# Performance work log

Hardware: AMD Instinct MI355X
Metric: run time of the kernel (lower is better)

The kernel has to match this reference:

```python
import jax, jax.numpy as jnp
import numpy as np

N_NODES = 50000


def setup_inputs() -> dict:
    key = jax.random.key(0)
    k1, k2, k3, k4, k5 = jax.random.split(key, 5)
    x = jax.random.normal(k1, (N_NODES, 128), dtype=jnp.float32)
    edge_index = jax.random.randint(k2, (2, 800000), 0, N_NODES, dtype=jnp.int64)
    # Linear layers: torch Linear stores weight as [out, in]; init ~ U(-1/sqrt(in), 1/sqrt(in))
    s = 1.0 / np.sqrt(128.0)
    W_rel = jax.random.uniform(k3, (128, 128), dtype=jnp.float32, minval=-s, maxval=s)
    b_rel = jax.random.uniform(k4, (128,), dtype=jnp.float32, minval=-s, maxval=s)
    W_root = jax.random.uniform(k5, (128, 128), dtype=jnp.float32, minval=-s, maxval=s)
    return {"x": x, "edge_index": edge_index, "W_rel": W_rel, "b_rel": b_rel, "W_root": W_root}


def reference(x, edge_index, W_rel, b_rel, W_root):
    # GraphConv (PyG): out_i = W_rel @ (sum_{j -> i} x_j) + b_rel + W_root @ x_i
    src, dst = edge_index[0], edge_index[1]
    msgs = x[src]  # [E, in] gather
    agg = jax.ops.segment_sum(msgs, dst, num_segments=N_NODES)  # [N, in] scatter-add
    out = agg @ W_rel.T + b_rel + x @ W_root.T
    # ReLU; dropout_rate = DropoutRate.NONE -> p=0, identity
    return jax.nn.relu(out)
```

## Files before the change

kernel.cpp:

```cpp
#include <hip/hip_runtime.h>
#include <hip/hip_bf16.h>


#define F 128
#define NPB 32
#define NPARTS 8
#define CAPLOG 7
#define CAP (1 << CAPLOG)
#define CAPB 768
#define SCAN_CHUNK 2048

typedef __bf16 bf16x8 __attribute__((ext_vector_type(8)));
typedef float f32x4 __attribute__((ext_vector_type(4)));

__device__ inline unsigned f32_to_bf16_rne(float f) {
  unsigned u = __float_as_uint(f);
  unsigned r = u + 0x7fffu + ((u >> 16) & 1u);
  return r >> 16;
}

__global__ __launch_bounds__(256) void convert_bf16_kernel(
    const float2* __restrict__ in, unsigned* __restrict__ out, int n2) {
  int i = blockIdx.x * blockDim.x + threadIdx.x;
  int stride = gridDim.x * blockDim.x;
  for (; i < n2; i += stride) {
    float2 v = in[i];
    out[i] = f32_to_bf16_rne(v.x) | (f32_to_bf16_rne(v.y) << 16);
  }
}

__global__ __launch_bounds__(256) void bin_kernel(
    const int* __restrict__ ei, int* __restrict__ binCursor,
    unsigned* __restrict__ bin, int E, int NB) {
  const int part = blockIdx.x & (NPARTS - 1);
  const int stride = gridDim.x * blockDim.x;
  for (int e = blockIdx.x * blockDim.x + threadIdx.x; e < E; e += stride) {
    unsigned src = (unsigned)ei[e];
    unsigned dst = (unsigned)ei[E + e];
    unsigned key = (dst << 16) | src;
    int cell = part * NB + (int)(dst >> 5);
    int slot = atomicAdd(&binCursor[cell], 1);
    if (slot < CAP) bin[((size_t)cell << CAPLOG) + slot] = key;
  }
}

__global__ __launch_bounds__(256) void agg_sort_kernel(
    const unsigned* __restrict__ xb, const unsigned* __restrict__ bin,
    const int* __restrict__ binCursor, unsigned* __restrict__ aggb,
    int N, int NB) {
  __shared__ int cntS[NPB];
  __shared__ int offS[NPB];
  __shared__ int curS[NPB];
  __shared__ unsigned short eLds[CAPB];
  const int b = blockIdx.x;
  const int t = threadIdx.x;

  if (t < NPB) cntS[t] = 0;
  __syncthreads();

  unsigned kreg[NPARTS];
  int cnt_p[NPARTS];
#pragma unroll
  for (int p = 0; p < NPARTS; ++p) {
    int cell = p * NB + b;
    int c = min(binCursor[cell], CAP);
    cnt_p[p] = c;
    if (t < c) {
      kreg[p] = bin[((size_t)cell << CAPLOG) + t];
      atomicAdd(&cntS[(kreg[p] >> 16) & (NPB - 1)], 1);
    }
  }
  __syncthreads();

  if (t < 64) {
    int v = (t < NPB) ? cntS[t] : 0;
    int incl = v;
#pragma unroll
    for (int off = 1; off < NPB; off <<= 1) {
      int u = __shfl_up(incl, off);
      if (t >= off) incl += u;
    }
    if (t < NPB) {
      offS[t] = incl - v;
      curS[t] = incl - v;
    }
  }
  __syncthreads();

#pragma unroll
  for (int p = 0; p < NPARTS; ++p) {
    if (t < cnt_p[p]) {
      int d = (kreg[p] >> 16) & (NPB - 1);
      int pos = atomicAdd(&curS[d], 1);
      if (pos < CAPB) eLds[pos] = (unsigned short)(kreg[p] & 0xffffu);
    }
  }
  __syncthreads();

  const int wave = t >> 6;
  const int lane = t & 63;
  const int nodeBase = b * NPB;
  for (int di = wave; di < NPB; di += 4) {
    int node = nodeBase + di;
    if (node >= N) continue;
    int beg = min(offS[di], CAPB);
    int end = min(offS[di] + cntS[di], CAPB);
    float ax = 0.f, ay = 0.f;
    int e = beg;
    for (; e + 3 < end; e += 4) {
      int s0 = eLds[e + 0];
      int s1 = eLds[e + 1];
      int s2 = eLds[e + 2];
      int s3 = eLds[e + 3];
      unsigned v0 = xb[(size_t)s0 * 64 + lane];
      unsigned v1 = xb[(size_t)s1 * 64 + lane];
      unsigned v2 = xb[(size_t)s2 * 64 + lane];
      unsigned v3 = xb[(size_t)s3 * 64 + lane];
      ax += __uint_as_float(v0 << 16);
      ay += __uint_as_float(v0 & 0xffff0000u);
      ax += __uint_as_float(v1 << 16);
      ay += __uint_as_float(v1 & 0xffff0000u);
      ax += __uint_as_float(v2 << 16);
      ay += __uint_as_float(v2 & 0xffff0000u);
      ax += __uint_as_float(v3 << 16);
      ay += __uint_as_float(v3 & 0xffff0000u);
    }
    for (; e < end; ++e) {
      unsigned v = xb[(size_t)eLds[e] * 64 + lane];
      ax += __uint_as_float(v << 16);
      ay += __uint_as_float(v & 0xffff0000u);
    }
    aggb[(size_t)node * 64 + lane] = f32_to_bf16_rne(ax) | (f32_to_bf16_rne(ay) << 16);
  }
}

__global__ __launch_bounds__(256) void gemm_mfma_kernel(
    const __bf16* __restrict__ aggb, const __bf16* __restrict__ xb,
    const __bf16* __restrict__ wb,
    const float* __restrict__ brel, float* __restrict__ out, int N) {
  const int wave = threadIdx.x >> 6;
  const int lane = threadIdx.x & 63;
  const int m16 = lane & 15;
  const int quad = lane >> 4;
  const int rowBase = blockIdx.x * 128 + wave * 32;

  const f32x4 zero4 = {0.f, 0.f, 0.f, 0.f};
  f32x4 acc[2][8];
#pragma unroll
  for (int mt = 0; mt < 2; ++mt)
#pragma unroll
    for (int nt = 0; nt < 8; ++nt) acc[mt][nt] = zero4;

  const bf16x8 zero8 = {};

#pragma unroll
  for (int ph = 0; ph < 2; ++ph) {
    const __bf16* __restrict__ A = ph ? xb : aggb;
    const __bf16* __restrict__ W = wb + (size_t)ph * 128 * 128;
#pragma unroll
    for (int k0 = 0; k0 < 128; k0 += 32) {
      const int kcol = k0 + 8 * quad;
      bf16x8 a[2], bfr[8];
#pragma unroll
      for (int mt = 0; mt < 2; ++mt) {
        int row = rowBase + mt * 16 + m16;
        a[mt] = (row < N) ? *(const bf16x8*)(A + (size_t)row * F + kcol) : zero8;
      }
#pragma unroll
      for (int nt = 0; nt < 8; ++nt)
        bfr[nt] = *(const bf16x8*)(W + (size_t)(nt * 16 + m16) * F + kcol);
#pragma unroll
      for (int mt = 0; mt < 2; ++mt)
#pragma unroll
        for (int nt = 0; nt < 8; ++nt)
          acc[mt][nt] = __builtin_amdgcn_mfma_f32_16x16x32_bf16(
              a[mt], bfr[nt], acc[mt][nt], 0, 0, 0);
    }
  }

#pragma unroll
  for (int nt = 0; nt < 8; ++nt) {
    float bias = brel[nt * 16 + m16];
#pragma unroll
    for (int mt = 0; mt < 2; ++mt) {
      int row0 = rowBase + mt * 16 + quad * 4;
#pragma unroll
      for (int r = 0; r < 4; ++r) {
        int row = row0 + r;
        if (row < N)
          out[(size_t)row * F + nt * 16 + m16] = fmaxf(acc[mt][nt][r] + bias, 0.f);
      }
    }
  }
}

__global__ __launch_bounds__(256) void hist_kernel(
    const int* __restrict__ ei, int* __restrict__ counts, int E) {
  int e = blockIdx.x * blockDim.x + threadIdx.x;
  if (e < E) atomicAdd(&counts[ei[E + e]], 1);
}

__global__ __launch_bounds__(256) void scanA_kernel(
    const int* __restrict__ counts, int* __restrict__ blockSums, int N) {
  __shared__ int red[256];
  int base = blockIdx.x * SCAN_CHUNK;
  int sum = 0;
  for (int i = threadIdx.x; i < SCAN_CHUNK; i += 256) {
    int idx = base + i;
    if (idx < N) sum += counts[idx];
  }
  red[threadIdx.x] = sum;
  __syncthreads();
#pragma unroll
  for (int off = 128; off > 0; off >>= 1) {
    if (threadIdx.x < off) red[threadIdx.x] += red[threadIdx.x + off];
    __syncthreads();
  }
  if (threadIdx.x == 0) blockSums[blockIdx.x] = red[0];
}

__global__ __launch_bounds__(64) void scanB_kernel(
    const int* __restrict__ blockSums, int* __restrict__ blockOffsets,
    int nb, int* __restrict__ offsets, int N, int E) {
  int lane = threadIdx.x;
  int orig = (lane < nb) ? blockSums[lane] : 0;
  int v = orig;
#pragma unroll
  for (int off = 1; off < 64; off <<= 1) {
    int u = __shfl_up(v, off);
    if (lane >= off) v += u;
  }
  if (lane < nb) blockOffsets[lane] = v - orig;
  if (lane == 0) offsets[N] = E;
}

__global__ __launch_bounds__(256) void scanC_kernel(
    const int* __restrict__ counts, const int* __restrict__ blockOffsets,
    int* __restrict__ offsets, int* __restrict__ cursor, int N) {
  __shared__ int tsum[256];
  const int t = threadIdx.x;
  int base = blockIdx.x * SCAN_CHUNK + t * 8;
  int c[8];
  int s = 0;
#pragma unroll
  for (int i = 0; i < 8; ++i) {
    int idx = base + i;
    c[i] = (idx < N) ? counts[idx] : 0;
    s += c[i];
  }
  tsum[t] = s;
  __syncthreads();
  for (int off = 1; off < 256; off <<= 1) {
    int u = (t >= off) ? tsum[t - off] : 0;
    __syncthreads();
    tsum[t] += u;
    __syncthreads();
  }
  int pre = blockOffsets[blockIdx.x] + tsum[t] - s;
#pragma unroll
  for (int i = 0; i < 8; ++i) {
    int idx = base + i;
    if (idx < N) {
      offsets[idx] = pre;
      cursor[idx] = pre;
      pre += c[i];
    }
  }
}

__global__ __launch_bounds__(256) void build_kernel(
    const int* __restrict__ ei, int* __restrict__ cursor,
    int* __restrict__ edge_src, int E) {
  int e = blockIdx.x * blockDim.x + threadIdx.x;
  if (e < E) {
    int dst = ei[E + e];
    int pos = atomicAdd(&cursor[dst], 1);
    edge_src[pos] = ei[e];
  }
}

__global__ __launch_bounds__(256) void aggregate_bf16_kernel(
    const unsigned* __restrict__ xb, const int* __restrict__ edge_src,
    const int* __restrict__ offsets, unsigned* __restrict__ aggb, int N) {
  int node = blockIdx.x * 4 + (threadIdx.x >> 6);
  if (node >= N) return;
  int lane = threadIdx.x & 63;
  int beg = offsets[node];
  int end = offsets[node + 1];
  float ax = 0.f, ay = 0.f;
  int e = beg;
  for (; e + 4 <= end; e += 4) {
    unsigned v0 = xb[(size_t)edge_src[e + 0] * 64 + lane];
    unsigned v1 = xb[(size_t)edge_src[e + 1] * 64 + lane];
    unsigned v2 = xb[(size_t)edge_src[e + 2] * 64 + lane];
    unsigned v3 = xb[(size_t)edge_src[e + 3] * 64 + lane];
    ax += __uint_as_float(v0 << 16);
    ay += __uint_as_float(v0 & 0xffff0000u);
    ax += __uint_as_float(v1 << 16);
    ay += __uint_as_float(v1 & 0xffff0000u);
    ax += __uint_as_float(v2 << 16);
    ay += __uint_as_float(v2 & 0xffff0000u);
    ax += __uint_as_float(v3 << 16);
    ay += __uint_as_float(v3 & 0xffff0000u);
  }
  for (; e < end; ++e) {
    unsigned v = xb[(size_t)edge_src[e] * 64 + lane];
    ax += __uint_as_float(v << 16);
    ay += __uint_as_float(v & 0xffff0000u);
  }
  aggb[(size_t)node * 64 + lane] = f32_to_bf16_rne(ax) | (f32_to_bf16_rne(ay) << 16);
}

__global__ __launch_bounds__(256) void scatter_add_kernel(
    const float4* __restrict__ x4, const int* __restrict__ ei,
    float* __restrict__ agg, int E) {
  int gid = blockIdx.x * blockDim.x + threadIdx.x;
  if (gid >= E * 32) return;
  int e = gid >> 5, q = gid & 31;
  float4 v = x4[(size_t)ei[e] * 32 + q];
  float* a = agg + (size_t)ei[E + e] * F + q * 4;
  atomicAdd(a + 0, v.x);
  atomicAdd(a + 1, v.y);
  atomicAdd(a + 2, v.z);
  atomicAdd(a + 3, v.w);
}

#define ROWS_PER_BLOCK 64
#define SA_STRIDE 36
#define SW_STRIDE 132

__global__ __launch_bounds__(256) void gemm_fused_kernel(
    const float* __restrict__ agg, const float* __restrict__ x,
    const float* __restrict__ Wrel, const float* __restrict__ Wroot,
    const float* __restrict__ brel, float* __restrict__ out, int N) {
  __shared__ float sA[ROWS_PER_BLOCK * SA_STRIDE];
  __shared__ float sW[32 * SW_STRIDE];
  const int tid = threadIdx.x;
  const int j0 = (tid & 31) * 4;
  const int r0 = (tid >> 5) * 8;
  const int rowBase = blockIdx.x * ROWS_PER_BLOCK;
  float acc[8][4];
#pragma unroll
  for (int r = 0; r < 8; ++r)
#pragma unroll
    for (int c = 0; c < 4; ++c) acc[r][c] = 0.0f;
  for (int phase = 0; phase < 2; ++phase) {
    const float* __restrict__ A = phase ? x : agg;
    const float* __restrict__ W = phase ? Wroot : Wrel;
    for (int kc = 0; kc < F; kc += 32) {
#pragma unroll
      for (int idx = tid; idx < 512; idx += 256) {
        int row = idx >> 3, k4 = idx & 7;
        float4 v = make_float4(0.f, 0.f, 0.f, 0.f);
        int grow = rowBase + row;
        if (grow < N) v = *(const float4*)&A[(size_t)grow * F + kc + k4 * 4];
        *(float4*)&sA[row * SA_STRIDE + k4 * 4] = v;
      }
#pragma unroll
      for (int idx = tid; idx < 4096; idx += 256) {
        int j = idx >> 5, kk = idx & 31;
        sW[kk * SW_STRIDE + j] = W[j * F + kc + kk];
      }
      __syncthreads();
#pragma unroll
      for (int kk = 0; kk < 32; ++kk) {
        float4 w = *(const float4*)&sW[kk * SW_STRIDE + j0];
#pragma unroll
        for (int r = 0; r < 8; ++r) {
          float a = sA[(r0 + r) * SA_STRIDE + kk];
          acc[r][0] = fmaf(a, w.x, acc[r][0]);
          acc[r][1] = fmaf(a, w.y, acc[r][1]);
          acc[r][2] = fmaf(a, w.z, acc[r][2]);
          acc[r][3] = fmaf(a, w.w, acc[r][3]);
        }
      }
      __syncthreads();
    }
  }
  float b0 = brel[j0], b1 = brel[j0 + 1], b2 = brel[j0 + 2], b3 = brel[j0 + 3];
#pragma unroll
  for (int r = 0; r < 8; ++r) {
    int row = rowBase + r0 + r;
    if (row < N) {
      float4 v;
      v.x = fmaxf(acc[r][0] + b0, 0.0f);
      v.y = fmaxf(acc[r][1] + b1, 0.0f);
      v.z = fmaxf(acc[r][2] + b2, 0.0f);
      v.w = fmaxf(acc[r][3] + b3, 0.0f);
      *(float4*)&out[(size_t)row * F + j0] = v;
    }
  }
}

extern "C" void kernel_launch(void* const* d_in, const int* in_sizes, int n_in,
                              void* d_out, int out_size, void* d_ws, size_t ws_size,
                              hipStream_t stream) {
  const float* x     = (const float*)d_in[0];
  const int*   ei    = (const int*)d_in[1];
  const float* Wrel  = (const float*)d_in[2];
  const float* brel  = (const float*)d_in[3];
  const float* Wroot = (const float*)d_in[4];
  float* out = (float*)d_out;

  const int N = in_sizes[0] / F;
  const int E = in_sizes[1] / 2;

  size_t xbBytes = ((size_t)N * F * 2 + 255) & ~(size_t)255;
  size_t wBytes  = ((size_t)2 * F * F * 2 + 255) & ~(size_t)255;

  const int NB = (N + NPB - 1) / NPB;
  size_t curBytes = ((size_t)NPARTS * NB * sizeof(int) + 255) & ~(size_t)255;
  size_t binBytes = ((size_t)NPARTS * NB * CAP * sizeof(unsigned) + 255) & ~(size_t)255;
  size_t needBin = curBytes + binBytes + xbBytes + wBytes + xbBytes;

  const int nbs = (N + SCAN_CHUNK - 1) / SCAN_CHUNK;
  size_t intBytes =
      ((size_t)(E + 3 * N + 1 + 2 * nbs) * sizeof(int) + 255) & ~(size_t)255;
  size_t needCsr = intBytes + xbBytes + wBytes + xbBytes;

  if (ws_size >= needBin) {
    int*      binCursor = (int*)d_ws;
    unsigned* bin  = (unsigned*)((char*)d_ws + curBytes);
    unsigned* xb   = (unsigned*)((char*)d_ws + curBytes + binBytes);
    __bf16*   wb   = (__bf16*)((char*)d_ws + curBytes + binBytes + xbBytes);
    unsigned* aggb = (unsigned*)((char*)d_ws + curBytes + binBytes + xbBytes + wBytes);

    hipMemsetAsync(binCursor, 0, (size_t)NPARTS * NB * sizeof(int), stream);
    convert_bf16_kernel<<<2048, 256, 0, stream>>>((const float2*)x, xb, N * 64);
    convert_bf16_kernel<<<32, 256, 0, stream>>>((const float2*)Wrel,
                                                (unsigned*)wb, F * F / 2);
    convert_bf16_kernel<<<32, 256, 0, stream>>>(
        (const float2*)Wroot, (unsigned*)(wb + F * F), F * F / 2);

    bin_kernel<<<1024, 256, 0, stream>>>(ei, binCursor, bin, E, NB);
    agg_sort_kernel<<<NB, 256, 0, stream>>>(xb, bin, binCursor, aggb, N, NB);
    gemm_mfma_kernel<<<(N + 127) / 128, 256, 0, stream>>>(
        (const __bf16*)aggb, (const __bf16*)xb, wb, brel, out, N);
  } else if (ws_size >= needCsr) {
    int* edge_src  = (int*)d_ws;
    int* counts    = edge_src + E;
    int* offsets   = counts + N;
    int* cursor    = offsets + N + 1;
    int* blockSums = cursor + N;
    int* blockOffs = blockSums + nbs;
    unsigned* xb   = (unsigned*)((char*)d_ws + intBytes);
    __bf16*   wb   = (__bf16*)((char*)d_ws + intBytes + xbBytes);
    unsigned* aggb = (unsigned*)((char*)d_ws + intBytes + xbBytes + wBytes);

    hipMemsetAsync(counts, 0, (size_t)N * sizeof(int), stream);
    convert_bf16_kernel<<<2048, 256, 0, stream>>>((const float2*)x, xb, N * 64);
    convert_bf16_kernel<<<32, 256, 0, stream>>>((const float2*)Wrel,
                                                (unsigned*)wb, F * F / 2);
    convert_bf16_kernel<<<32, 256, 0, stream>>>(
        (const float2*)Wroot, (unsigned*)(wb + F * F), F * F / 2);
    hist_kernel<<<(E + 255) / 256, 256, 0, stream>>>(ei, counts, E);
    scanA_kernel<<<nbs, 256, 0, stream>>>(counts, blockSums, N);
    scanB_kernel<<<1, 64, 0, stream>>>(blockSums, blockOffs, nbs, offsets, N, E);
    scanC_kernel<<<nbs, 256, 0, stream>>>(counts, blockOffs, offsets, cursor, N);
    build_kernel<<<(E + 255) / 256, 256, 0, stream>>>(ei, cursor, edge_src, E);
    aggregate_bf16_kernel<<<(N + 3) / 4, 256, 0, stream>>>(xb, edge_src, offsets,
                                                           aggb, N);
    gemm_mfma_kernel<<<(N + 127) / 128, 256, 0, stream>>>(
        (const __bf16*)aggb, (const __bf16*)xb, wb, brel, out, N);
  } else {
    hipMemsetAsync(out, 0, (size_t)N * F * sizeof(float), stream);
    long long total = (long long)E * 32;
    scatter_add_kernel<<<(int)((total + 255) / 256), 256, 0, stream>>>(
        (const float4*)x, ei, out, E);
    gemm_fused_kernel<<<(N + ROWS_PER_BLOCK - 1) / ROWS_PER_BLOCK, 256, 0,
                        stream>>>(out, x, Wrel, Wroot, brel, out, N);
  }
}
```

Measured before the change: 189.9 us.

## Fuse aggregation with MFMA GEMM and merge prep conversions into one kernel

```diff
diff --git a/kernel.cpp b/kernel.cpp
--- a/kernel.cpp
+++ b/kernel.cpp
@@ -8,6 +8,7 @@
 #define CAPLOG 7
 #define CAP (1 << CAPLOG)
 #define CAPB 768
+#define AST 68
 #define SCAN_CHUNK 2048
 
 typedef __bf16 bf16x8 __attribute__((ext_vector_type(8)));
@@ -18,14 +19,30 @@
   unsigned r = u + 0x7fffu + ((u >> 16) & 1u);
   return r >> 16;
 }
-
-__global__ __launch_bounds__(256) void convert_bf16_kernel(
-    const float2* __restrict__ in, unsigned* __restrict__ out, int n2) {
+__device__ inline unsigned pack2(float2 v) {
+  return f32_to_bf16_rne(v.x) | (f32_to_bf16_rne(v.y) << 16);
+}
+
+__global__ __launch_bounds__(256) void prep_kernel(
+    const float2* __restrict__ x, const float2* __restrict__ w0,
+    const float2* __restrict__ w1, unsigned* __restrict__ xb,
+    unsigned* __restrict__ wb, int* __restrict__ binCursor,
+    int n2x, int n2w, int ncur) {
   int i = blockIdx.x * blockDim.x + threadIdx.x;
-  int stride = gridDim.x * blockDim.x;
-  for (; i < n2; i += stride) {
-    float2 v = in[i];
-    out[i] = f32_to_bf16_rne(v.x) | (f32_to_bf16_rne(v.y) << 16);
+  const int stride = gridDim.x * blockDim.x;
+  const int total = n2x + 2 * n2w + ncur;
+  for (; i < total; i += stride) {
+    if (i < n2x) {
+      xb[i] = pack2(x[i]);
+    } else if (i < n2x + n2w) {
+      int j = i - n2x;
+      wb[j] = pack2(w0[j]);
+    } else if (i < n2x + 2 * n2w) {
+      int j = i - n2x - n2w;
+      wb[n2w + j] = pack2(w1[j]);
+    } else {
+      binCursor[i - n2x - 2 * n2w] = 0;
+    }
   }
 }
 
@@ -44,14 +61,15 @@
   }
 }
 
-__global__ __launch_bounds__(256) void agg_sort_kernel(
+__global__ __launch_bounds__(256) void agg_gemm_kernel(
     const unsigned* __restrict__ xb, const unsigned* __restrict__ bin,
-    const int* __restrict__ binCursor, unsigned* __restrict__ aggb,
-    int N, int NB) {
+    const int* __restrict__ binCursor, const __bf16* __restrict__ wb,
+    const float* __restrict__ brel, float* __restrict__ out, int N, int NB) {
   __shared__ int cntS[NPB];
   __shared__ int offS[NPB];
   __shared__ int curS[NPB];
   __shared__ unsigned short eLds[CAPB];
+  __shared__ unsigned aLds[NPB * AST];
   const int b = blockIdx.x;
   const int t = threadIdx.x;
 
@@ -102,96 +120,103 @@
   const int nodeBase = b * NPB;
   for (int di = wave; di < NPB; di += 4) {
     int node = nodeBase + di;
-    if (node >= N) continue;
-    int beg = min(offS[di], CAPB);
-    int end = min(offS[di] + cntS[di], CAPB);
     float ax = 0.f, ay = 0.f;
-    int e = beg;
-    for (; e + 3 < end; e += 4) {
-      int s0 = eLds[e + 0];
-      int s1 = eLds[e + 1];
-      int s2 = eLds[e + 2];
-      int s3 = eLds[e + 3];
-      unsigned v0 = xb[(size_t)s0 * 64 + lane];
-      unsigned v1 = xb[(size_t)s1 * 64 + lane];
-      unsigned v2 = xb[(size_t)s2 * 64 + lane];
-      unsigned v3 = xb[(size_t)s3 * 64 + lane];
-      ax += __uint_as_float(v0 << 16);
-      ay += __uint_as_float(v0 & 0xffff0000u);
-      ax += __uint_as_float(v1 << 16);
-      ay += __uint_as_float(v1 & 0xffff0000u);
-      ax += __uint_as_float(v2 << 16);
-      ay += __uint_as_float(v2 & 0xffff0000u);
-      ax += __uint_as_float(v3 << 16);
-      ay += __uint_as_float(v3 & 0xffff0000u);
-    }
-    for (; e < end; ++e) {
-      unsigned v = xb[(size_t)eLds[e] * 64 + lane];
-      ax += __uint_as_float(v << 16);
-      ay += __uint_as_float(v & 0xffff0000u);
-    }
-    aggb[(size_t)node * 64 + lane] = f32_to_bf16_rne(ax) | (f32_to_bf16_rne(ay) << 16);
-  }
-}
-
-__global__ __launch_bounds__(256) void gemm_mfma_kernel(
-    const __bf16* __restrict__ aggb, const __bf16* __restrict__ xb,
-    const __bf16* __restrict__ wb,
-    const float* __restrict__ brel, float* __restrict__ out, int N) {
-  const int wave = threadIdx.x >> 6;
-  const int lane = threadIdx.x & 63;
+    if (node < N) {
+      int beg = min(offS[di], CAPB);
+      int end = min(offS[di] + cntS[di], CAPB);
+      int e = beg;
+      for (; e + 3 < end; e += 4) {
+        int s0 = eLds[e + 0];
+        int s1 = eLds[e + 1];
+        int s2 = eLds[e + 2];
+        int s3 = eLds[e + 3];
+        unsigned v0 = xb[(size_t)s0 * 64 + lane];
+        unsigned v1 = xb[(size_t)s1 * 64 + lane];
+        unsigned v2 = xb[(size_t)s2 * 64 + lane];
+        unsigned v3 = xb[(size_t)s3 * 64 + lane];
+        ax += __uint_as_float(v0 << 16);
+        ay += __uint_as_float(v0 & 0xffff0000u);
+        ax += __uint_as_float(v1 << 16);
+        ay += __uint_as_float(v1 & 0xffff0000u);
+        ax += __uint_as_float(v2 << 16);
+        ay += __uint_as_float(v2 & 0xffff0000u);
+        ax += __uint_as_float(v3 << 16);
+        ay += __uint_as_float(v3 & 0xffff0000u);
+      }
+      for (; e < end; ++e) {
+        unsigned v = xb[(size_t)eLds[e] * 64 + lane];
+        ax += __uint_as_float(v << 16);
+        ay += __uint_as_float(v & 0xffff0000u);
+      }
+    }
+    aLds[di * AST + lane] = f32_to_bf16_rne(ax) | (f32_to_bf16_rne(ay) << 16);
+  }
+  __syncthreads();
+
   const int m16 = lane & 15;
   const int quad = lane >> 4;
-  const int rowBase = blockIdx.x * 128 + wave * 32;
-
   const f32x4 zero4 = {0.f, 0.f, 0.f, 0.f};
-  f32x4 acc[2][8];
+  const bf16x8 zero8 = {};
+  f32x4 acc[2][2];
 #pragma unroll
   for (int mt = 0; mt < 2; ++mt)
 #pragma unroll
-    for (int nt = 0; nt < 8; ++nt) acc[mt][nt] = zero4;
-
-  const bf16x8 zero8 = {};
+    for (int s = 0; s < 2; ++s) acc[mt][s] = zero4;
 
 #pragma unroll
   for (int ph = 0; ph < 2; ++ph) {
-    const __bf16* __restrict__ A = ph ? xb : aggb;
-    const __bf16* __restrict__ W = wb + (size_t)ph * 128 * 128;
-#pragma unroll
-    for (int k0 = 0; k0 < 128; k0 += 32) {
+    const __bf16* __restrict__ W = wb + (size_t)ph * F * F;
+#pragma unroll
+    for (int k0 = 0; k0 < F; k0 += 32) {
       const int kcol = k0 + 8 * quad;
-      bf16x8 a[2], bfr[8];
+      bf16x8 a[2], bw[2];
 #pragma unroll
       for (int mt = 0; mt < 2; ++mt) {
-        int row = rowBase + mt * 16 + m16;
-        a[mt] = (row < N) ? *(const bf16x8*)(A + (size_t)row * F + kcol) : zero8;
-      }
-#pragma unroll
-      for (int nt = 0; nt < 8; ++nt)
-        bfr[nt] = *(const bf16x8*)(W + (size_t)(nt * 16 + m16) * F + kcol);
+        if (ph == 0) {
+          a[mt] = *(const bf16x8*)&aLds[(mt * 16 + m16) * AST + (kcol >> 1)];
+        } else {
+          int row = nodeBase + mt * 16 + m16;
+          a[mt] = (row < N)
+                      ? *(const bf16x8*)((const __bf16*)xb + (size_t)row * F + kcol)
+                      : zero8;
+        }
+      }
+#pragma unroll
+      for (int s = 0; s < 2; ++s) {
+        int nt = wave * 2 + s;
+        bw[s] = *(const bf16x8*)(W + (size_t)(nt * 16 + m16) * F + kcol);
+      }
 #pragma unroll
       for (int mt = 0; mt < 2; ++mt)
 #pragma unroll
-        for (int nt = 0; nt < 8; ++nt)
-          acc[mt][nt] = __builtin_amdgcn_mfma_f32_16x16x32_bf16(
-              a[mt], bfr[nt], acc[mt][nt], 0, 0, 0);
-    }
-  }
-
-#pragma unroll
-  for (int nt = 0; nt < 8; ++nt) {
+        for (int s = 0; s < 2; ++s)
+          acc[mt][s] = __builtin_amdgcn_mfma_f32_16x16x32_bf16(
+              a[mt], bw[s], acc[mt][s], 0, 0, 0);
+    }
+  }
+
+#pragma unroll
+  for (int s = 0; s < 2; ++s) {
+    int nt = wave * 2 + s;
     float bias = brel[nt * 16 + m16];
 #pragma unroll
     for (int mt = 0; mt < 2; ++mt) {
-      int row0 = rowBase + mt * 16 + quad * 4;
+      int row0 = nodeBase + mt * 16 + quad * 4;
 #pragma unroll
       for (int r = 0; r < 4; ++r) {
         int row = row0 + r;
         if (row < N)
-          out[(size_t)row * F + nt * 16 + m16] = fmaxf(acc[mt][nt][r] + bias, 0.f);
-      }
-    }
-  }
+          out[(size_t)row * F + nt * 16 + m16] = fmaxf(acc[mt][s][r] + bias, 0.f);
+      }
+    }
+  }
+}
+
+__global__ __launch_bounds__(256) void convert_bf16_kernel(
+    const float2* __restrict__ in, unsigned* __restrict__ out, int n2) {
+  int i = blockIdx.x * blockDim.x + threadIdx.x;
+  int stride = gridDim.x * blockDim.x;
+  for (; i < n2; i += stride) out[i] = pack2(in[i]);
 }
 
 __global__ __launch_bounds__(256) void hist_kernel(
@@ -311,6 +336,62 @@
   aggb[(size_t)node * 64 + lane] = f32_to_bf16_rne(ax) | (f32_to_bf16_rne(ay) << 16);
 }
 
+__global__ __launch_bounds__(256) void gemm_mfma_kernel(
+    const __bf16* __restrict__ aggb, const __bf16* __restrict__ xb,
+    const __bf16* __restrict__ wb, const float* __restrict__ brel,
+    float* __restrict__ out, int N) {
+  const int wave = threadIdx.x >> 6;
+  const int lane = threadIdx.x & 63;
+  const int m16 = lane & 15;
+  const int quad = lane >> 4;
+  const int rowBase = blockIdx.x * 128 + wave * 32;
+  const f32x4 zero4 = {0.f, 0.f, 0.f, 0.f};
+  f32x4 acc[2][8];
+#pragma unroll
+  for (int mt = 0; mt < 2; ++mt)
+#pragma unroll
+    for (int nt = 0; nt < 8; ++nt) acc[mt][nt] = zero4;
+  const bf16x8 zero8 = {};
+#pragma unroll
+  for (int ph = 0; ph < 2; ++ph) {
+    const __bf16* __restrict__ A = ph ? xb : aggb;
+    const __bf16* __restrict__ W = wb + (size_t)ph * 128 * 128;
+#pragma unroll
+    for (int k0 = 0; k0 < 128; k0 += 32) {
+      const int kcol = k0 + 8 * quad;
+      bf16x8 a[2], bfr[8];
+#pragma unroll
+      for (int mt = 0; mt < 2; ++mt) {
+        int row = rowBase + mt * 16 + m16;
+        a[mt] = (row < N) ? *(const bf16x8*)(A + (size_t)row * F + kcol) : zero8;
+      }
+#pragma unroll
+      for (int nt = 0; nt < 8; ++nt)
+        bfr[nt] = *(const bf16x8*)(W + (size_t)(nt * 16 + m16) * F + kcol);
+#pragma unroll
+      for (int mt = 0; mt < 2; ++mt)
+#pragma unroll
+        for (int nt = 0; nt < 8; ++nt)
+          acc[mt][nt] = __builtin_amdgcn_mfma_f32_16x16x32_bf16(
+              a[mt], bfr[nt], acc[mt][nt], 0, 0, 0);
+    }
+  }
+#pragma unroll
+  for (int nt = 0; nt < 8; ++nt) {
+    float bias = brel[nt * 16 + m16];
+#pragma unroll
+    for (int mt = 0; mt < 2; ++mt) {
+      int row0 = rowBase + mt * 16 + quad * 4;
+#pragma unroll
+      for (int r = 0; r < 4; ++r) {
+        int row = row0 + r;
+        if (row < N)
+          out[(size_t)row * F + nt * 16 + m16] = fmaxf(acc[mt][nt][r] + bias, 0.f);
+      }
+    }
+  }
+}
+
 __global__ __launch_bounds__(256) void scatter_add_kernel(
     const float4* __restrict__ x4, const int* __restrict__ ei,
     float* __restrict__ agg, int E) {
@@ -411,7 +492,7 @@
   const int NB = (N + NPB - 1) / NPB;
   size_t curBytes = ((size_t)NPARTS * NB * sizeof(int) + 255) & ~(size_t)255;
   size_t binBytes = ((size_t)NPARTS * NB * CAP * sizeof(unsigned) + 255) & ~(size_t)255;
-  size_t needBin = curBytes + binBytes + xbBytes + wBytes + xbBytes;
+  size_t needBin = curBytes + binBytes + xbBytes + wBytes;
 
   const int nbs = (N + SCAN_CHUNK - 1) / SCAN_CHUNK;
   size_t intBytes =
@@ -420,22 +501,18 @@
 
   if (ws_size >= needBin) {
     int*      binCursor = (int*)d_ws;
-    unsigned* bin  = (unsigned*)((char*)d_ws + curBytes);
-    unsigned* xb   = (unsigned*)((char*)d_ws + curBytes + binBytes);
-    __bf16*   wb   = (__bf16*)((char*)d_ws + curBytes + binBytes + xbBytes);
-    unsigned* aggb = (unsigned*)((char*)d_ws + curBytes + binBytes + xbBytes + wBytes);
-
-    hipMemsetAsync(binCursor, 0, (size_t)NPARTS * NB * sizeof(int), stream);
-    convert_bf16_kernel<<<2048, 256, 0, stream>>>((const float2*)x, xb, N * 64);
-    convert_bf16_kernel<<<32, 256, 0, stream>>>((const float2*)Wrel,
-                                                (unsigned*)wb, F * F / 2);
-    convert_bf16_kernel<<<32, 256, 0, stream>>>(
-        (const float2*)Wroot, (unsigned*)(wb + F * F), F * F / 2);
-
+    unsigned* bin = (unsigned*)((char*)d_ws + curBytes);
+    unsigned* xb  = (unsigned*)((char*)d_ws + curBytes + binBytes);
+    unsigned* wb  = (unsigned*)((char*)d_ws + curBytes + binBytes + xbBytes);
+
+    const int n2x = N * (F / 2);
+    const int n2w = F * F / 2;
+    prep_kernel<<<2048, 256, 0, stream>>>((const float2*)x, (const float2*)Wrel,
+                                          (const float2*)Wroot, xb, wb, binCursor,
+                                          n2x, n2w, NPARTS * NB);
     bin_kernel<<<1024, 256, 0, stream>>>(ei, binCursor, bin, E, NB);
-    agg_sort_kernel<<<NB, 256, 0, stream>>>(xb, bin, binCursor, aggb, N, NB);
-    gemm_mfma_kernel<<<(N + 127) / 128, 256, 0, stream>>>(
-        (const __bf16*)aggb, (const __bf16*)xb, wb, brel, out, N);
+    agg_gemm_kernel<<<NB, 256, 0, stream>>>(xb, bin, binCursor,
+                                            (const __bf16*)wb, brel, out, N, NB);
   } else if (ws_size >= needCsr) {
     int* edge_src  = (int*)d_ws;
     int* counts    = edge_src + E;
@@ -461,7 +538,7 @@
     aggregate_bf16_kernel<<<(N + 3) / 4, 256, 0, stream>>>(xb, edge_src, offsets,
                                                            aggb, N);
     gemm_mfma_kernel<<<(N + 127) / 128, 256, 0, stream>>>(
-        (const __bf16*)aggb, (const __bf16*)xb, wb, brel, out, N);
+        (const __bf16*)aggb, (const __bf16*)xb, (const __bf16*)wb, brel, out, N);
   } else {
     hipMemsetAsync(out, 0, (size_t)N * F * sizeof(float), stream);
     long long total = (long long)E * 32;
```

New measurement: 173.0 us. 8.9% less time.
